# Kernel tuning notes

Measured on AMD Instinct MI355X. Metric: run time of the kernel, lower is better.

The kernel has to match this reference:

```python
import jax, jax.numpy as jnp
import numpy as np

N_NODES = 100000


def gcn_conv(x, W, b, src, dst, n):
    # PyG GCNConv: linear transform, add self-loops, symmetric degree norm, scatter-add, bias
    h = x @ W                                      # [n, d_out]
    loop = jnp.arange(n, dtype=src.dtype)
    s = jnp.concatenate([src, loop])               # [E + n]
    d = jnp.concatenate([dst, loop])
    deg = jax.ops.segment_sum(jnp.ones_like(d, dtype=h.dtype), d, num_segments=n)
    dinv = jnp.where(deg > 0, jax.lax.rsqrt(deg), 0.0)
    norm = dinv[s] * dinv[d]                       # [E + n]
    msg = h[s] * norm[:, None]                     # gather + scale
    out = jax.ops.segment_sum(msg, d, num_segments=n)  # scatter-add over targets
    return out + b


def setup_inputs() -> dict:
    key = jax.random.key(0)
    ks = jax.random.split(key, 8)
    n, c_in, hid, c_out = N_NODES, 256, 128, 64
    x = jax.random.normal(ks[0], (n, c_in), dtype=jnp.float32)
    edge_index = jax.random.randint(ks[1], (2, 1600000), 0, n, dtype=jnp.int64)
    s = 0.1
    return {
        "x": x,
        "edge_index": edge_index,
        "W1": jax.random.normal(ks[2], (c_in, hid), dtype=jnp.float32) * s,
        "b1": jnp.zeros((hid,), dtype=jnp.float32),
        "Wmu": jax.random.normal(ks[3], (hid, c_out), dtype=jnp.float32) * s,
        "bmu": jnp.zeros((c_out,), dtype=jnp.float32),
        "Wlv": jax.random.normal(ks[4], (hid, c_out), dtype=jnp.float32) * s,
        "blv": jnp.zeros((c_out,), dtype=jnp.float32),
    }


def reference(x, edge_index, W1, b1, Wmu, bmu, Wlv, blv):
    n = x.shape[0]
    src, dst = edge_index[0], edge_index[1]
    h = jax.nn.relu(gcn_conv(x, W1, b1, src, dst, n))
    mu = gcn_conv(h, Wmu, bmu, src, dst, n)
    logvar = gcn_conv(h, Wlv, blv, src, dst, n)
    return mu, logvar
```

## Files before the change

### kernel.cpp

```cpp
#include <hip/hip_runtime.h>


#define C_IN  256
#define HID   128
#define C_OUT 64
#define NBUCK 1024
#define P1WGS 256

typedef __attribute__((ext_vector_type(8))) short bf16x8;
typedef __attribute__((ext_vector_type(4))) float f32x4;

__device__ inline unsigned short f2bf(float f) {
  unsigned u = __float_as_uint(f);
  unsigned r = u + 0x7FFF + ((u >> 16) & 1);
  return (unsigned short)(r >> 16);
}
__device__ inline float bflo(unsigned v) { return __uint_as_float(v << 16); }
__device__ inline float bfhi(unsigned v) { return __uint_as_float(v & 0xFFFF0000u); }

__global__ __launch_bounds__(256) void k_bin_count(const int* __restrict__ dst,
                                                   int* __restrict__ histmat, int E) {
  __shared__ int h[NBUCK];
  int tid = threadIdx.x;
  for (int i = tid; i < NBUCK; i += 256) h[i] = 0;
  __syncthreads();
  for (int e = blockIdx.x * 256 + tid; e < E; e += P1WGS * 256)
    atomicAdd(&h[dst[e] >> 7], 1);
  __syncthreads();
  for (int i = tid; i < NBUCK; i += 256)
    histmat[blockIdx.x * NBUCK + i] = h[i];
}

__global__ __launch_bounds__(256) void k_col_scan(int* __restrict__ histmat,
                                                  int* __restrict__ bucket_tot) {
  __shared__ int sh[P1WGS];
  int b = blockIdx.x;
  int t = threadIdx.x;
  int v = histmat[t * NBUCK + b];
  sh[t] = v; __syncthreads();
  for (int ofs = 1; ofs < P1WGS; ofs <<= 1) {
    int add = (t >= ofs) ? sh[t - ofs] : 0;
    __syncthreads();
    sh[t] += add;
    __syncthreads();
  }
  histmat[t * NBUCK + b] = sh[t] - v;
  if (t == P1WGS - 1) bucket_tot[b] = sh[t];
}

__global__ void k_bucket_scan(const int* __restrict__ bucket_tot,
                              int* __restrict__ bucket_start, int E) {
  __shared__ int sh[NBUCK];
  int t = threadIdx.x;
  int v = bucket_tot[t];
  sh[t] = v; __syncthreads();
  for (int ofs = 1; ofs < NBUCK; ofs <<= 1) {
    int add = (t >= ofs) ? sh[t - ofs] : 0;
    __syncthreads();
    sh[t] += add;
    __syncthreads();
  }
  bucket_start[t] = sh[t] - v;
  if (t == NBUCK - 1) bucket_start[NBUCK] = E;
}

__global__ __launch_bounds__(256) void k_bin_scatter(const int* __restrict__ src,
                                                     const int* __restrict__ dst,
                                                     const int* __restrict__ histmat,
                                                     const int* __restrict__ bucket_start,
                                                     unsigned* __restrict__ binned, int E) {
  __shared__ int cur[NBUCK];
  int tid = threadIdx.x;
  for (int i = tid; i < NBUCK; i += 256)
    cur[i] = bucket_start[i] + histmat[blockIdx.x * NBUCK + i];
  __syncthreads();
  for (int e = blockIdx.x * 256 + tid; e < E; e += P1WGS * 256) {
    int d = dst[e];
    int pos = atomicAdd(&cur[d >> 7], 1);
    binned[pos] = (unsigned)src[e] | ((unsigned)(d & 127) << 17);
  }
}

__global__ __launch_bounds__(256) void k_bucket_csr(const unsigned* __restrict__ binned,
                                                    const int* __restrict__ bucket_start,
                                                    int* __restrict__ row_start,
                                                    float* __restrict__ dinv,
                                                    int* __restrict__ csr_src,
                                                    int n, int E) {
  __shared__ int h[128], ls[128], c[128];
  int b = blockIdx.x, t = threadIdx.x;
  int start = bucket_start[b], end = bucket_start[b + 1];
  if (t < 128) h[t] = 0;
  __syncthreads();
  for (int e = start + t; e < end; e += 256)
    atomicAdd(&h[binned[e] >> 17], 1);
  __syncthreads();
  if (t < 128) ls[t] = h[t];
  __syncthreads();
  for (int ofs = 1; ofs < 128; ofs <<= 1) {
    int add = (t < 128 && t >= ofs) ? ls[t - ofs] : 0;
    __syncthreads();
    if (t < 128) ls[t] += add;
    __syncthreads();
  }
  if (t < 128) {
    int excl = ls[t] - h[t];
    ls[t] = excl;
    c[t] = excl;
    int node = b * 128 + t;
    if (node < n) {
      row_start[node] = start + excl;
      dinv[node] = rsqrtf((float)h[t] + 1.0f);
    }
  }
  if (b == 0 && t == 0) row_start[n] = E;
  __syncthreads();
  for (int e = start + t; e < end; e += 256) {
    unsigned v = binned[e];
    int pos = start + atomicAdd(&c[v >> 17], 1);
    csr_src[pos] = (int)(v & 0x1FFFF);
  }
}

__global__ void k_prep(const float* __restrict__ W1, const float* __restrict__ Wmu,
                       const float* __restrict__ Wlv,
                       unsigned short* __restrict__ bswz1,
                       unsigned short* __restrict__ bswz2,
                       unsigned* __restrict__ p1d, unsigned* __restrict__ p2d,
                       int rows) {
  int idx = blockIdx.x * 256 + threadIdx.x;
  if (idx < 4096) {
    int L = idx & 63, t = (idx >> 6) & 7, s = idx >> 9;
    const float* srcp = W1 + (size_t)(s * 32 + ((L >> 4) << 3)) * 128 + t * 16 + (L & 15);
    unsigned short* dstp = bswz1 + (size_t)idx * 8;
#pragma unroll
    for (int j = 0; j < 8; j++) dstp[j] = f2bf(srcp[(size_t)j * 128]);
  } else if (idx < 6144) {
    int id2 = idx - 4096;
    int L = id2 & 63, t = (id2 >> 6) & 7, s = id2 >> 9;
    int nn = t * 16 + (L & 15);
    int k0 = s * 32 + ((L >> 4) << 3);
    const float* W = (nn < C_OUT) ? (Wmu + nn) : (Wlv + (nn - C_OUT));
    unsigned short* dstp = bswz2 + (size_t)id2 * 8;
#pragma unroll
    for (int j = 0; j < 8; j++) dstp[j] = f2bf(W[(size_t)(k0 + j) * C_OUT]);
  } else if (idx < 6208) {
    int j = idx - 6144;
    p1d[((size_t)(j >> 3) * rows + (rows - 1)) * 8 + (j & 7)] = 0u;
  } else if (idx < 6272) {
    int j = idx - 6208;
    p2d[((size_t)(j >> 3) * rows + (rows - 1)) * 8 + (j & 7)] = 0u;
  }
}

template <typename AT, int K>
__global__ __launch_bounds__(256) void k_gemm_mfma(const AT* __restrict__ A,
                                                   const unsigned short* __restrict__ bswz,
                                                   unsigned short* __restrict__ C,
                                                   const float* __restrict__ dinv,
                                                   int M, int rows) {
  constexpr int NS = K / 32;
  int wave = threadIdx.x >> 6, lane = threadIdx.x & 63;
  int m0 = blockIdx.x * 64 + wave * 16;
  int lrow = lane & 15, lq = lane >> 4;
  int arow = m0 + lrow;
  bool rv = arow < M;
  int arow_c = rv ? arow : 0;

  auto loadA = [&](int s) -> bf16x8 {
    if (sizeof(AT) == 4) {
      const float* af = (const float*)A + (size_t)arow_c * K + lq * 8 + s * 32;
      float4 u0 = rv ? *(const float4*)(af) : float4{0, 0, 0, 0};
      float4 u1 = rv ? *(const float4*)(af + 4) : float4{0, 0, 0, 0};
      union { unsigned short us[8]; bf16x8 v; } tmp;
      tmp.us[0] = f2bf(u0.x); tmp.us[1] = f2bf(u0.y);
      tmp.us[2] = f2bf(u0.z); tmp.us[3] = f2bf(u0.w);
      tmp.us[4] = f2bf(u1.x); tmp.us[5] = f2bf(u1.y);
      tmp.us[6] = f2bf(u1.z); tmp.us[7] = f2bf(u1.w);
      return tmp.v;
    } else {
      int c0 = lq * 8 + s * 32;
      const unsigned short* ab = (const unsigned short*)A +
          ((size_t)(c0 >> 4) * rows + arow_c) * 16 + (c0 & 15);
      return rv ? *(const bf16x8*)(ab) : (bf16x8)(short)0;
    }
  };

  f32x4 acc[8];
#pragma unroll
  for (int t = 0; t < 8; t++) acc[t] = (f32x4){0.f, 0.f, 0.f, 0.f};

  bf16x8 a_cur = loadA(0);
  bf16x8 b_cur[8];
#pragma unroll
  for (int t = 0; t < 8; t++)
    b_cur[t] = *(const bf16x8*)(bswz + lane * 8 + t * 512);

#pragma unroll
  for (int s = 0; s < NS; ++s) {
    bf16x8 a_nxt = a_cur;
    bf16x8 b_nxt[8];
    if (s + 1 < NS) {
      a_nxt = loadA(s + 1);
      const unsigned short* bp = bswz + (size_t)(s + 1) * 4096 + lane * 8;
#pragma unroll
      for (int t = 0; t < 8; t++) b_nxt[t] = *(const bf16x8*)(bp + t * 512);
    }
#pragma unroll
    for (int t = 0; t < 8; t++)
      acc[t] = __builtin_amdgcn_mfma_f32_16x16x32_bf16(a_cur, b_cur[t], acc[t], 0, 0, 0);
    a_cur = a_nxt;
    if (s + 1 < NS) {
#pragma unroll
      for (int t = 0; t < 8; t++) b_cur[t] = b_nxt[t];
    }
  }
#pragma unroll
  for (int i = 0; i < 4; i++) {
    int rr = m0 + lq * 4 + i;
    if (rr < M) {
      float dsc = dinv[rr];
#pragma unroll
      for (int t = 0; t < 8; t++)
        C[((size_t)t * rows + rr) * 16 + lrow] = f2bf(acc[t][i] * dsc);
    }
  }
}

__device__ __forceinline__ void gather_slice(const unsigned* __restrict__ psl,
                                             const int* __restrict__ csr,
                                             int n, int node, int rs, int re,
                                             int maxcnt, int li, int vb,
                                             float& a0, float& a1) {
  a0 = 0.f; a1 = 0.f;
  for (int t0 = 0; t0 < maxcnt; t0 += 8) {
    int s = rs + t0 + li;
    int sl = n;
    if (s < re) sl = csr[s];
    else if (s == re) sl = node;
    int km = maxcnt - t0; if (km > 8) km = 8;
    for (int k = 0; k < km; k += 4) {
      int sk0 = __builtin_amdgcn_ds_bpermute(vb + ((k + 0) << 2), sl);
      int sk1 = __builtin_amdgcn_ds_bpermute(vb + ((k + 1) << 2), sl);
      int sk2 = __builtin_amdgcn_ds_bpermute(vb + ((k + 2) << 2), sl);
      int sk3 = __builtin_amdgcn_ds_bpermute(vb + ((k + 3) << 2), sl);
      unsigned v0 = psl[(((unsigned)sk0) << 3) + li];
      unsigned v1 = psl[(((unsigned)sk1) << 3) + li];
      unsigned v2 = psl[(((unsigned)sk2) << 3) + li];
      unsigned v3 = psl[(((unsigned)sk3) << 3) + li];
      a0 += bflo(v0); a1 += bfhi(v0);
      a0 += bflo(v1); a1 += bfhi(v1);
      a0 += bflo(v2); a1 += bfhi(v2);
      a0 += bflo(v3); a1 += bfhi(v3);
    }
  }
}

#define AGG_SLICE_SETUP                                                             \
  int tid = threadIdx.x;                                                            \
  int slice = blockIdx.x & 7;                       \
  int nb = blockIdx.x >> 3;                                                         \
  int lane = tid & 63;                                                              \
  int li = lane & 7;                                \
  int node = nb * 32 + (tid >> 6) * 8 + (lane >> 3);                                \
  int rs = 0, re = -1;                                                              \
  if (node < n) { rs = row_start[node]; re = row_start[node + 1]; }                 \
  int mc = re - rs + 1;                                       \
  mc = max(mc, __shfl_xor(mc, 8, 64));                                              \
  mc = max(mc, __shfl_xor(mc, 16, 64));                                             \
  mc = max(mc, __shfl_xor(mc, 32, 64));                                             \
  int maxcnt = __builtin_amdgcn_readfirstlane(mc);                                  \
  const unsigned* psl = (const unsigned*)p + (size_t)slice * (n + 1) * 8;           \
  int vb = (lane & 56) << 2;     \
  float a0, a1;                                                                     \
  gather_slice(psl, csr, n, node, rs, re, maxcnt, li, vb, a0, a1);

__global__ __launch_bounds__(256) void k_agg_relu_bf(
    const unsigned short* __restrict__ p, const float* __restrict__ dinv,
    const int* __restrict__ row_start, const int* __restrict__ csr,
    const float* __restrict__ bias, unsigned short* __restrict__ h, int n) {
  AGG_SLICE_SETUP
  if (node < n) {
    float di = dinv[node];
    float2 bb = *(const float2*)(bias + slice * 16 + li * 2);
    float r0 = fmaxf(a0 * di + bb.x, 0.f);
    float r1 = fmaxf(a1 * di + bb.y, 0.f);
    unsigned pk = (unsigned)f2bf(r0) | ((unsigned)f2bf(r1) << 16);
    ((unsigned*)h)[((size_t)slice * (n + 1) + node) * 8 + li] = pk;
  }
}

__global__ __launch_bounds__(256) void k_agg_out_bf(
    const unsigned short* __restrict__ p, const float* __restrict__ dinv,
    const int* __restrict__ row_start, const int* __restrict__ csr,
    const float* __restrict__ bmu, const float* __restrict__ blv,
    float* __restrict__ out, int n) {
  AGG_SLICE_SETUP
  if (node < n) {
    float di = dinv[node];
    const float* bp = (slice < 4) ? (bmu + slice * 16 + li * 2)
                                  : (blv + (slice - 4) * 16 + li * 2);
    float* op = (slice < 4)
                    ? (out + (size_t)node * C_OUT + slice * 16 + li * 2)
                    : (out + (size_t)(n + node) * C_OUT + (slice - 4) * 16 + li * 2);
    float2 bb = *(const float2*)bp;
    float2 res = {a0 * di + bb.x, a1 * di + bb.y};
    *(float2*)op = res;
  }
}

extern "C" void kernel_launch(void* const* d_in, const int* in_sizes, int n_in,
                              void* d_out, int out_size, void* d_ws, size_t ws_size,
                              hipStream_t stream) {
  const float* x   = (const float*)d_in[0];
  const int*   ei  = (const int*)d_in[1];
  const float* W1  = (const float*)d_in[2];
  const float* b1  = (const float*)d_in[3];
  const float* Wmu = (const float*)d_in[4];
  const float* bmu = (const float*)d_in[5];
  const float* Wlv = (const float*)d_in[6];
  const float* blv = (const float*)d_in[7];
  float* out = (float*)d_out;

  const int n = in_sizes[0] / C_IN;
  const int E = in_sizes[1] / 2;
  const int* src = ei;
  const int* dst = ei + E;

  char* w = (char*)d_ws;
  auto alloc = [&](size_t bytes) -> void* {
    void* pp = (void*)w;
    w += (bytes + 255) & ~(size_t)255;
    return pp;
  };
  float*          dinv       = (float*)alloc((size_t)n * 4);
  int*            row_start  = (int*)alloc((size_t)(n + 1) * 4);
  int*            histmat    = (int*)alloc((size_t)P1WGS * NBUCK * 4);
  int*            bucket_tot = (int*)alloc((size_t)NBUCK * 4);
  int*            bucket_st  = (int*)alloc((size_t)(NBUCK + 1) * 4);
  unsigned*       binned     = (unsigned*)alloc((size_t)E * 4);
  int*            csr_src    = (int*)alloc((size_t)E * 4);
  unsigned short* bswz1      = (unsigned short*)alloc((size_t)C_IN * 128 * 2);
  unsigned short* bswz2      = (unsigned short*)alloc((size_t)HID * 128 * 2);
  unsigned short* p1         = (unsigned short*)alloc((size_t)(n + 1) * 128 * 2);
  unsigned short* hbuf       = (unsigned short*)alloc((size_t)(n + 1) * 128 * 2);
  unsigned short* p2         = (unsigned short*)alloc((size_t)(n + 1) * 128 * 2);
  (void)ws_size; (void)n_in; (void)out_size;

  const int TB = 256;
  const int rows = n + 1;
  const int gemm_bks = (n + 63) / 64;
  const int agg_bks = ((n + 31) / 32) * 8;
  const int nbk_csr = (n + 127) / 128;

  k_bin_count<<<P1WGS, TB, 0, stream>>>(dst, histmat, E);
  k_col_scan<<<NBUCK, TB, 0, stream>>>(histmat, bucket_tot);
  k_bucket_scan<<<1, NBUCK, 0, stream>>>(bucket_tot, bucket_st, E);
  k_bin_scatter<<<P1WGS, TB, 0, stream>>>(src, dst, histmat, bucket_st, binned, E);
  k_bucket_csr<<<nbk_csr, TB, 0, stream>>>(binned, bucket_st, row_start, dinv,
                                           csr_src, n, E);

  k_prep<<<25, 256, 0, stream>>>(W1, Wmu, Wlv, bswz1, bswz2,
                                 (unsigned*)p1, (unsigned*)p2, rows);

  k_gemm_mfma<float, C_IN><<<gemm_bks, TB, 0, stream>>>(x, bswz1, p1, dinv, n, rows);
  k_agg_relu_bf<<<agg_bks, TB, 0, stream>>>(p1, dinv, row_start, csr_src, b1, hbuf, n);

  k_gemm_mfma<unsigned short, HID><<<gemm_bks, TB, 0, stream>>>(hbuf, bswz2, p2, dinv, n, rows);
  k_agg_out_bf<<<agg_bks, TB, 0, stream>>>(p2, dinv, row_start, csr_src, bmu, blv, out, n);
}
```

Before: 440.7 us.

## Pad CSR rows to multiples of four and vectorize pull aggregation

The CSR build is split into a degree pass, a second scan over padded bucket totals, and a fill pass that pads each row to a multiple of four with a dummy index pointing at the zero row n. The aggregation kernels now give four threads per node, each owning four features. Each thread loads four neighbour indices with one uint4 read and gathers uint2 feature chunks, instead of using wave-wide bpermute broadcasts bounded by the per-group maximum degree. The self-loop is added explicitly afterwards. This removes the load imbalance from max-degree loops and the shuffle overhead. In exchange it adds an extra kernel launch and scan, a larger CSR buffer, and wasted gathers on padding entries.

After: 461.0 us. 1.05x slower.

```diff
diff --git a/kernel.cpp b/kernel.cpp
--- a/kernel.cpp
+++ b/kernel.cpp
@@ -48,11 +48,10 @@
   if (t == P1WGS - 1) bucket_tot[b] = sh[t];
 }
 
-__global__ void k_bucket_scan(const int* __restrict__ bucket_tot,
-                              int* __restrict__ bucket_start, int E) {
+__global__ void k_scan(const int* __restrict__ tot, int* __restrict__ startv) {
   __shared__ int sh[NBUCK];
   int t = threadIdx.x;
-  int v = bucket_tot[t];
+  int v = tot[t];
   sh[t] = v; __syncthreads();
   for (int ofs = 1; ofs < NBUCK; ofs <<= 1) {
     int add = (t >= ofs) ? sh[t - ofs] : 0;
@@ -60,8 +59,8 @@
     sh[t] += add;
     __syncthreads();
   }
-  bucket_start[t] = sh[t] - v;
-  if (t == NBUCK - 1) bucket_start[NBUCK] = E;
+  startv[t] = sh[t] - v;
+  if (t == NBUCK - 1) startv[NBUCK] = sh[t];
 }
 
 __global__ __launch_bounds__(256) void k_bin_scatter(const int* __restrict__ src,
@@ -81,21 +80,21 @@
   }
 }
 
-__global__ __launch_bounds__(256) void k_bucket_csr(const unsigned* __restrict__ binned,
-                                                    const int* __restrict__ bucket_start,
-                                                    int* __restrict__ row_start,
+__global__ __launch_bounds__(256) void k_bucket_deg(const unsigned* __restrict__ binned,
+                                                    const int* __restrict__ bucket_st,
                                                     float* __restrict__ dinv,
-                                                    int* __restrict__ csr_src,
-                                                    int n, int E) {
-  __shared__ int h[128], ls[128], c[128];
+                                                    int* __restrict__ prow_start,
+                                                    int* __restrict__ pbtot, int n) {
+  __shared__ int h[128], ls[128];
   int b = blockIdx.x, t = threadIdx.x;
-  int start = bucket_start[b], end = bucket_start[b + 1];
+  int start = bucket_st[b], end = bucket_st[b + 1];
   if (t < 128) h[t] = 0;
   __syncthreads();
   for (int e = start + t; e < end; e += 256)
     atomicAdd(&h[binned[e] >> 17], 1);
   __syncthreads();
-  if (t < 128) ls[t] = h[t];
+  int pd = 0;
+  if (t < 128) { pd = (h[t] + 3) & ~3; ls[t] = pd; }
   __syncthreads();
   for (int ofs = 1; ofs < 128; ofs <<= 1) {
     int add = (t < 128 && t >= ofs) ? ls[t - ofs] : 0;
@@ -104,21 +103,41 @@
     __syncthreads();
   }
   if (t < 128) {
-    int excl = ls[t] - h[t];
-    ls[t] = excl;
-    c[t] = excl;
     int node = b * 128 + t;
     if (node < n) {
-      row_start[node] = start + excl;
       dinv[node] = rsqrtf((float)h[t] + 1.0f);
-    }
-  }
-  if (b == 0 && t == 0) row_start[n] = E;
+      prow_start[node] = ls[t] - pd;
+    }
+    if (t == 127) pbtot[b] = ls[127];
+  }
+}
+
+__global__ __launch_bounds__(256) void k_csr_fill(const unsigned* __restrict__ binned,
+                                                  const int* __restrict__ bucket_st,
+                                                  const int* __restrict__ pbstart,
+                                                  int* __restrict__ prow_start,
+                                                  int* __restrict__ csr, int n) {
+  __shared__ int c[128];
+  int b = blockIdx.x, t = threadIdx.x;
+  int start = bucket_st[b], end = bucket_st[b + 1];
+  int pbs = pbstart[b];
+  int node = b * 128 + t;
+  if (t < 128 && node < n) {
+    int g = pbs + prow_start[node];
+    prow_start[node] = g;
+    c[t] = g;
+  }
+  if (b == 0 && t == 0) prow_start[n] = pbstart[NBUCK];
   __syncthreads();
   for (int e = start + t; e < end; e += 256) {
     unsigned v = binned[e];
-    int pos = start + atomicAdd(&c[v >> 17], 1);
-    csr_src[pos] = (int)(v & 0x1FFFF);
+    int pos = atomicAdd(&c[v >> 17], 1);
+    csr[pos] = (int)(v & 0x1FFFF);
+  }
+  __syncthreads();
+  if (t < 128 && node < n) {
+    int cur = c[t];
+    while (cur & 3) csr[cur++] = n;
   }
 }
 
@@ -227,85 +246,66 @@
   }
 }
 
-__device__ __forceinline__ void gather_slice(const unsigned* __restrict__ psl,
-                                             const int* __restrict__ csr,
-                                             int n, int node, int rs, int re,
-                                             int maxcnt, int li, int vb,
-                                             float& a0, float& a1) {
-  a0 = 0.f; a1 = 0.f;
-  for (int t0 = 0; t0 < maxcnt; t0 += 8) {
-    int s = rs + t0 + li;
-    int sl = n;
-    if (s < re) sl = csr[s];
-    else if (s == re) sl = node;
-    int km = maxcnt - t0; if (km > 8) km = 8;
-    for (int k = 0; k < km; k += 4) {
-      int sk0 = __builtin_amdgcn_ds_bpermute(vb + ((k + 0) << 2), sl);
-      int sk1 = __builtin_amdgcn_ds_bpermute(vb + ((k + 1) << 2), sl);
-      int sk2 = __builtin_amdgcn_ds_bpermute(vb + ((k + 2) << 2), sl);
-      int sk3 = __builtin_amdgcn_ds_bpermute(vb + ((k + 3) << 2), sl);
-      unsigned v0 = psl[(((unsigned)sk0) << 3) + li];
-      unsigned v1 = psl[(((unsigned)sk1) << 3) + li];
-      unsigned v2 = psl[(((unsigned)sk2) << 3) + li];
-      unsigned v3 = psl[(((unsigned)sk3) << 3) + li];
-      a0 += bflo(v0); a1 += bfhi(v0);
-      a0 += bflo(v1); a1 += bfhi(v1);
-      a0 += bflo(v2); a1 += bfhi(v2);
-      a0 += bflo(v3); a1 += bfhi(v3);
-    }
-  }
-}
-
-#define AGG_SLICE_SETUP                                                             \
+#define AGG_PULL_BODY                                                               \
   int tid = threadIdx.x;                                                            \
   int slice = blockIdx.x & 7;                       \
-  int nb = blockIdx.x >> 3;                                                         \
-  int lane = tid & 63;                                                              \
-  int li = lane & 7;                                \
-  int node = nb * 32 + (tid >> 6) * 8 + (lane >> 3);                                \
-  int rs = 0, re = -1;                                                              \
-  if (node < n) { rs = row_start[node]; re = row_start[node + 1]; }                 \
-  int mc = re - rs + 1;                                       \
-  mc = max(mc, __shfl_xor(mc, 8, 64));                                              \
-  mc = max(mc, __shfl_xor(mc, 16, 64));                                             \
-  mc = max(mc, __shfl_xor(mc, 32, 64));                                             \
-  int maxcnt = __builtin_amdgcn_readfirstlane(mc);                                  \
-  const unsigned* psl = (const unsigned*)p + (size_t)slice * (n + 1) * 8;           \
-  int vb = (lane & 56) << 2;     \
-  float a0, a1;                                                                     \
-  gather_slice(psl, csr, n, node, rs, re, maxcnt, li, vb, a0, a1);
+  int blk = blockIdx.x >> 3;                                                        \
+  int node = blk * 64 + (tid >> 2);                       \
+  int li = tid & 3;                                    \
+  bool valid = node < n;                                                            \
+  int rs = 0, re = 0;                                                               \
+  if (valid) { rs = prow_start[node]; re = prow_start[node + 1]; }                  \
+  const unsigned* psl = (const unsigned*)p + (size_t)slice * (size_t)(n + 1) * 8;   \
+  float a0 = 0.f, a1 = 0.f, a2 = 0.f, a3 = 0.f;                                     \
+  for (int e = rs; e < re; e += 4) {                                                \
+    uint4 se = *(const uint4*)(csr + e);                                            \
+    uint2 q0 = *(const uint2*)(psl + (unsigned)se.x * 8u + li * 2);                 \
+    uint2 q1 = *(const uint2*)(psl + (unsigned)se.y * 8u + li * 2);                 \
+    uint2 q2 = *(const uint2*)(psl + (unsigned)se.z * 8u + li * 2);                 \
+    uint2 q3 = *(const uint2*)(psl + (unsigned)se.w * 8u + li * 2);                 \
+    a0 += bflo(q0.x); a1 += bfhi(q0.x); a2 += bflo(q0.y); a3 += bfhi(q0.y);         \
+    a0 += bflo(q1.x); a1 += bfhi(q1.x); a2 += bflo(q1.y); a3 += bfhi(q1.y);         \
+    a0 += bflo(q2.x); a1 += bfhi(q2.x); a2 += bflo(q2.y); a3 += bfhi(q2.y);         \
+    a0 += bflo(q3.x); a1 += bfhi(q3.x); a2 += bflo(q3.y); a3 += bfhi(q3.y);         \
+  }
 
 __global__ __launch_bounds__(256) void k_agg_relu_bf(
     const unsigned short* __restrict__ p, const float* __restrict__ dinv,
-    const int* __restrict__ row_start, const int* __restrict__ csr,
+    const int* __restrict__ prow_start, const int* __restrict__ csr,
     const float* __restrict__ bias, unsigned short* __restrict__ h, int n) {
-  AGG_SLICE_SETUP
-  if (node < n) {
+  AGG_PULL_BODY
+  if (valid) {
     float di = dinv[node];
-    float2 bb = *(const float2*)(bias + slice * 16 + li * 2);
-    float r0 = fmaxf(a0 * di + bb.x, 0.f);
-    float r1 = fmaxf(a1 * di + bb.y, 0.f);
-    unsigned pk = (unsigned)f2bf(r0) | ((unsigned)f2bf(r1) << 16);
-    ((unsigned*)h)[((size_t)slice * (n + 1) + node) * 8 + li] = pk;
+    uint2 q = *(const uint2*)(psl + (unsigned)node * 8u + li * 2);
+    const float* bb = bias + slice * 16 + li * 4;
+    float r0 = fmaxf((a0 + bflo(q.x)) * di + bb[0], 0.f);
+    float r1 = fmaxf((a1 + bfhi(q.x)) * di + bb[1], 0.f);
+    float r2 = fmaxf((a2 + bflo(q.y)) * di + bb[2], 0.f);
+    float r3 = fmaxf((a3 + bfhi(q.y)) * di + bb[3], 0.f);
+    uint2 u;
+    u.x = (unsigned)f2bf(r0) | ((unsigned)f2bf(r1) << 16);
+    u.y = (unsigned)f2bf(r2) | ((unsigned)f2bf(r3) << 16);
+    *(uint2*)((unsigned*)h + ((size_t)slice * (n + 1) + node) * 8 + li * 2) = u;
   }
 }
 
 __global__ __launch_bounds__(256) void k_agg_out_bf(
     const unsigned short* __restrict__ p, const float* __restrict__ dinv,
-    const int* __restrict__ row_start, const int* __restrict__ csr,
+    const int* __restrict__ prow_start, const int* __restrict__ csr,
     const float* __restrict__ bmu, const float* __restrict__ blv,
     float* __restrict__ out, int n) {
-  AGG_SLICE_SETUP
-  if (node < n) {
+  AGG_PULL_BODY
+  if (valid) {
     float di = dinv[node];
-    const float* bp = (slice < 4) ? (bmu + slice * 16 + li * 2)
-                                  : (blv + (slice - 4) * 16 + li * 2);
+    uint2 q = *(const uint2*)(psl + (unsigned)node * 8u + li * 2);
+    const float* bp = (slice < 4) ? (bmu + slice * 16 + li * 4)
+                                  : (blv + (slice - 4) * 16 + li * 4);
     float* op = (slice < 4)
-                    ? (out + (size_t)node * C_OUT + slice * 16 + li * 2)
-                    : (out + (size_t)(n + node) * C_OUT + (slice - 4) * 16 + li * 2);
-    float2 bb = *(const float2*)bp;
-    float2 res = {a0 * di + bb.x, a1 * di + bb.y};
-    *(float2*)op = res;
+                    ? (out + (size_t)node * C_OUT + slice * 16 + li * 4)
+                    : (out + (size_t)(n + node) * C_OUT + (slice - 4) * 16 + li * 4);
+    float4 o = {(a0 + bflo(q.x)) * di + bp[0], (a1 + bfhi(q.x)) * di + bp[1],
+                (a2 + bflo(q.y)) * di + bp[2], (a3 + bfhi(q.y)) * di + bp[3]};
+    *(float4*)op = o;
   }
 }
 
@@ -334,12 +334,14 @@
     return pp;
   };
   float*          dinv       = (float*)alloc((size_t)n * 4);
-  int*            row_start  = (int*)alloc((size_t)(n + 1) * 4);
   int*            histmat    = (int*)alloc((size_t)P1WGS * NBUCK * 4);
   int*            bucket_tot = (int*)alloc((size_t)NBUCK * 4);
   int*            bucket_st  = (int*)alloc((size_t)(NBUCK + 1) * 4);
+  int*            pbtot      = (int*)alloc((size_t)NBUCK * 4);
+  int*            pbstart    = (int*)alloc((size_t)(NBUCK + 1) * 4);
   unsigned*       binned     = (unsigned*)alloc((size_t)E * 4);
-  int*            csr_src    = (int*)alloc((size_t)E * 4);
+  int*            prow_start = (int*)alloc((size_t)(n + 1) * 4);
+  int*            csr        = (int*)alloc(((size_t)E + 3 * n + 16) * 4);
   unsigned short* bswz1      = (unsigned short*)alloc((size_t)C_IN * 128 * 2);
   unsigned short* bswz2      = (unsigned short*)alloc((size_t)HID * 128 * 2);
   unsigned short* p1         = (unsigned short*)alloc((size_t)(n + 1) * 128 * 2);
@@ -350,22 +352,23 @@
   const int TB = 256;
   const int rows = n + 1;
   const int gemm_bks = (n + 63) / 64;
-  const int agg_bks = ((n + 31) / 32) * 8;
-  const int nbk_csr = (n + 127) / 128;
+  const int nbk = (n + 127) / 128;
+  const int agg_bks = ((n + 63) / 64) * 8;
 
   k_bin_count<<<P1WGS, TB, 0, stream>>>(dst, histmat, E);
   k_col_scan<<<NBUCK, TB, 0, stream>>>(histmat, bucket_tot);
-  k_bucket_scan<<<1, NBUCK, 0, stream>>>(bucket_tot, bucket_st, E);
+  k_scan<<<1, NBUCK, 0, stream>>>(bucket_tot, bucket_st);
   k_bin_scatter<<<P1WGS, TB, 0, stream>>>(src, dst, histmat, bucket_st, binned, E);
-  k_bucket_csr<<<nbk_csr, TB, 0, stream>>>(binned, bucket_st, row_start, dinv,
-                                           csr_src, n, E);
+  k_bucket_deg<<<NBUCK, TB, 0, stream>>>(binned, bucket_st, dinv, prow_start, pbtot, n);
+  k_scan<<<1, NBUCK, 0, stream>>>(pbtot, pbstart);
+  k_csr_fill<<<nbk, TB, 0, stream>>>(binned, bucket_st, pbstart, prow_start, csr, n);
 
   k_prep<<<25, 256, 0, stream>>>(W1, Wmu, Wlv, bswz1, bswz2,
                                  (unsigned*)p1, (unsigned*)p2, rows);
 
   k_gemm_mfma<float, C_IN><<<gemm_bks, TB, 0, stream>>>(x, bswz1, p1, dinv, n, rows);
-  k_agg_relu_bf<<<agg_bks, TB, 0, stream>>>(p1, dinv, row_start, csr_src, b1, hbuf, n);
+  k_agg_relu_bf<<<agg_bks, TB, 0, stream>>>(p1, dinv, prow_start, csr, b1, hbuf, n);
 
   k_gemm_mfma<unsigned short, HID><<<gemm_bks, TB, 0, stream>>>(hbuf, bswz2, p2, dinv, n, rows);
-  k_agg_out_bf<<<agg_bks, TB, 0, stream>>>(p2, dinv, row_start, csr_src, bmu, blv, out, n);
-}
+  k_agg_out_bf<<<agg_bks, TB, 0, stream>>>(p2, dinv, prow_start, csr, bmu, blv, out, n);
+}
```
